# Kernel optimization log

Measured on AMD Instinct MI355X. Metric: run time of the kernel, lower is better.

## Reference

```python
import jax, jax.numpy as jnp
import numpy as np

N_NODES = 100000
N_EDGES = 1600000
IN_F, HID_F, OUT_F = 128, 128, 64


def gcn_conv(x, edge_index, W, b):
    # x: [N, Fin]; W: [Fout, Fin] (torch Linear layout); b: [Fout]
    h = x @ W.T + b  # [N, Fout]
    src, dst = edge_index[0], edge_index[1]
    n = x.shape[0]
    # in-degree via scatter-add of ones on dst (matches torch code)
    deg = jax.ops.segment_sum(jnp.ones(src.shape[0], dtype=h.dtype), dst, num_segments=n)
    deg_inv_sqrt = jnp.where(deg > 0, deg ** -0.5, 0.0)
    w = deg_inv_sqrt[src] * deg_inv_sqrt[dst]  # edge_weight defaults to ones
    msg = w[:, None] * h[src]  # [E, Fout] gather + scale
    return jax.ops.segment_sum(msg, dst, num_segments=n)  # scatter-add aggregate


def setup_inputs() -> dict:
    key = jax.random.key(0)
    k1, k2, k3, k4 = jax.random.split(key, 4)
    x = jax.random.normal(k1, (N_NODES, IN_F), dtype=jnp.float32)
    edge_index = jax.random.randint(k2, (2, N_EDGES), 0, N_NODES, dtype=jnp.int64)
    # xavier-uniform-like weights, zero bias (torch Linear layout [out, in])
    lim1 = float(np.sqrt(6.0 / (IN_F + HID_F)))
    lim2 = float(np.sqrt(6.0 / (HID_F + OUT_F)))
    W1 = jax.random.uniform(k3, (HID_F, IN_F), jnp.float32, -lim1, lim1)
    W2 = jax.random.uniform(k4, (OUT_F, HID_F), jnp.float32, -lim2, lim2)
    b1 = jnp.zeros((HID_F,), jnp.float32)
    b2 = jnp.zeros((OUT_F,), jnp.float32)
    return {"x": x, "edge_index": edge_index, "W1": W1, "b1": b1, "W2": W2, "b2": b2}


def reference(x, edge_index, W1, b1, W2, b2):
    # layer 1 + relu (dropout is identity in eval mode)
    h = jax.nn.relu(gcn_conv(x, edge_index, W1, b1))
    # final layer, no activation
    return gcn_conv(h, edge_index, W2, b2)
```

## Files before the change

### kernel.cpp

```cpp
#include <hip/hip_runtime.h>

constexpr int FIN    = 128;
constexpr int LOG_RB = 7;
constexpr int RB     = 1 << LOG_RB;
constexpr int BMAX   = 1024;
constexpr int CAP    = 8192;
constexpr int CHUNK  = 4096;

typedef _Float16 half8 __attribute__((ext_vector_type(8)));
typedef float    f32x4 __attribute__((ext_vector_type(4)));

__global__ __launch_bounds__(1024) void init_gcur_kernel(int* __restrict__ gcur, int B) {
    int i = blockIdx.x * 1024 + threadIdx.x;
    if (i < B) gcur[i] = i * CAP;
}

__global__ __launch_bounds__(256) void bucket_scatter_kernel(
    const int* __restrict__ src, const int* __restrict__ dst,
    int* __restrict__ gcur, unsigned* __restrict__ gEdges, int E, int B)
{
    __shared__ int lhist[BMAX];
    __shared__ int lbase[BMAX];
    __shared__ int lcur[BMAX];
    const int e0 = blockIdx.x * CHUNK;
    const int e1 = min(e0 + CHUNK, E);
    for (int i = threadIdx.x; i < B; i += 256) { lhist[i] = 0; lcur[i] = 0; }
    __syncthreads();
    for (int e = e0 + threadIdx.x; e < e1; e += 256)
        atomicAdd(&lhist[dst[e] >> LOG_RB], 1);
    __syncthreads();
    for (int i = threadIdx.x; i < B; i += 256) {
        int c = lhist[i];
        if (c) lbase[i] = atomicAdd(&gcur[i], c);
    }
    __syncthreads();
    for (int e = e0 + threadIdx.x; e < e1; e += 256) {
        int d = dst[e];
        int b = d >> LOG_RB;
        int pos = lbase[b] + atomicAdd(&lcur[b], 1);
        if (pos < (b + 1) * CAP)
            gEdges[pos] = ((unsigned)src[e] << LOG_RB) | (unsigned)(d & (RB - 1));
    }
}

__global__ __launch_bounds__(256) void finalize_kernel(
    const unsigned* __restrict__ gEdges, const int* __restrict__ gcur,
    int* __restrict__ rbeg, int* __restrict__ rend, float* __restrict__ dis,
    int* __restrict__ esrc, int N)
{
    __shared__ int h[RB];
    __shared__ int excl[RB];
    __shared__ int cur[RB];
    const int b = blockIdx.x;
    const int base = b * CAP;
    int cnt = gcur[b] - base;
    if (cnt > CAP) cnt = CAP;
    const int node0 = b << LOG_RB;
    if (threadIdx.x < RB) h[threadIdx.x] = 0;
    __syncthreads();
    for (int i = threadIdx.x; i < cnt; i += 256)
        atomicAdd(&h[gEdges[base + i] & (RB - 1)], 1);
    __syncthreads();
    if (threadIdx.x < RB) excl[threadIdx.x] = h[threadIdx.x];
    __syncthreads();
    for (int off = 1; off < RB; off <<= 1) {
        int u = 0;
        if (threadIdx.x < RB && threadIdx.x >= off) u = excl[threadIdx.x - off];
        __syncthreads();
        if (threadIdx.x < RB) excl[threadIdx.x] += u;
        __syncthreads();
    }
    if (threadIdx.x < RB) {
        int c  = h[threadIdx.x];
        int ex = excl[threadIdx.x] - c;
        cur[threadIdx.x] = ex;
        int node = node0 + threadIdx.x;
        if (node < N) {
            rbeg[node] = base + ex;
            rend[node] = base + ex + c;
            dis[node]  = c > 0 ? rsqrtf((float)c) : 0.0f;
        }
    }
    __syncthreads();
    for (int i = threadIdx.x; i < cnt; i += 256) {
        unsigned p = gEdges[base + i];
        int dl = (int)(p & (RB - 1));
        int pos = base + atomicAdd(&cur[dl], 1);
        esrc[pos] = (int)(p >> LOG_RB);
    }
}

__global__ __launch_bounds__(256) void linear1_kernel(
    const float* __restrict__ X, const float* __restrict__ W,
    const float* __restrict__ Bv, const float* __restrict__ dis,
    _Float16* __restrict__ Y, int N)
{
    __shared__ __align__(16) _Float16 xs[64 * 128];
    const int tid  = threadIdx.x;
    const int wave = tid >> 6;
    const int lane = tid & 63;
    const int l15  = lane & 15;
    const int lhi  = lane >> 4;

    half8 wf[2][4];
    float bias[2];
    #pragma unroll
    for (int c = 0; c < 2; ++c) {
        int f = (wave * 2 + c) * 16 + l15;
        #pragma unroll
        for (int ks = 0; ks < 4; ++ks) {
            const float* wp = &W[f * 128 + ks * 32 + lhi * 8];
            float4 u0 = *(const float4*)wp;
            float4 u1 = *(const float4*)(wp + 4);
            half8 hh;
            hh[0] = (_Float16)u0.x; hh[1] = (_Float16)u0.y;
            hh[2] = (_Float16)u0.z; hh[3] = (_Float16)u0.w;
            hh[4] = (_Float16)u1.x; hh[5] = (_Float16)u1.y;
            hh[6] = (_Float16)u1.z; hh[7] = (_Float16)u1.w;
            wf[c][ks] = hh;
        }
        bias[c] = Bv[f];
    }

    const int nchunks = (N + 63) / 64;
    for (int ch = blockIdx.x; ch < nchunks; ch += gridDim.x) {
        const int n0 = ch * 64;
        __syncthreads();
        #pragma unroll
        for (int p = 0; p < 4; ++p) {
            int ci  = p * 256 + tid;
            int row = ci >> 4, c = ci & 15;
            int n   = n0 + row;
            int nc  = n < N ? n : N - 1;
            const float* xp = &X[(size_t)nc * 128 + c * 8];
            float4 u0 = *(const float4*)xp;
            float4 u1 = *(const float4*)(xp + 4);
            half8 hh;
            hh[0] = (_Float16)u0.x; hh[1] = (_Float16)u0.y;
            hh[2] = (_Float16)u0.z; hh[3] = (_Float16)u0.w;
            hh[4] = (_Float16)u1.x; hh[5] = (_Float16)u1.y;
            hh[6] = (_Float16)u1.z; hh[7] = (_Float16)u1.w;
            *(half8*)&xs[row * 128 + (c ^ (row & 7)) * 8] = hh;
        }
        __syncthreads();

        f32x4 acc[4][2];
        #pragma unroll
        for (int mt = 0; mt < 4; ++mt)
            #pragma unroll
            for (int c = 0; c < 2; ++c) {
                acc[mt][c][0] = bias[c]; acc[mt][c][1] = bias[c];
                acc[mt][c][2] = bias[c]; acc[mt][c][3] = bias[c];
            }

        #pragma unroll
        for (int mt = 0; mt < 4; ++mt) {
            int row = mt * 16 + l15;
            #pragma unroll
            for (int ks = 0; ks < 4; ++ks) {
                int c  = ks * 4 + lhi;
                half8 a = *(const half8*)&xs[row * 128 + (c ^ (row & 7)) * 8];
                #pragma unroll
                for (int c2 = 0; c2 < 2; ++c2)
                    acc[mt][c2] = __builtin_amdgcn_mfma_f32_16x16x32_f16(
                        a, wf[c2][ks], acc[mt][c2], 0, 0, 0);
            }
        }
        __syncthreads();
        #pragma unroll
        for (int mt = 0; mt < 4; ++mt)
            #pragma unroll
            for (int r = 0; r < 4; ++r) {
                int row = mt * 16 + lhi * 4 + r;
                int n   = n0 + row;
                int nc  = n < N ? n : N - 1;
                float dv = dis[nc];
                #pragma unroll
                for (int c2 = 0; c2 < 2; ++c2) {
                    int col = (wave * 2 + c2) * 16 + l15;
                    xs[row * 128 + col] = (_Float16)(dv * acc[mt][c2][r]);
                }
            }
        __syncthreads();
        #pragma unroll
        for (int p = 0; p < 4; ++p) {
            int ci  = p * 256 + tid;
            int row = ci >> 4, c = ci & 15;
            int n   = n0 + row;
            if (n < N)
                *(half8*)&Y[(size_t)n * 128 + c * 8] = *(const half8*)&xs[row * 128 + c * 8];
        }
    }
}

__global__ __launch_bounds__(256) void agg_lin2_kernel(
    const _Float16* __restrict__ H, const int* __restrict__ rbeg,
    const int* __restrict__ rend, const int* __restrict__ esrc,
    const float* __restrict__ dis, const float* __restrict__ W2,
    const float* __restrict__ b2, _Float16* __restrict__ h2, int N)
{
    __shared__ __align__(16) _Float16 tile[16 * 128];
    const int tid  = threadIdx.x;
    const int wave = tid >> 6;
    const int lane = tid & 63;
    const int l15  = lane & 15;
    const int lhi  = lane >> 4;
    const int rlane = tid & 15;
    const int rrow  = tid >> 4;

    half8 wf[4];
    float bias;
    {
        int f = wave * 16 + l15;
        #pragma unroll
        for (int ks = 0; ks < 4; ++ks) {
            const float* wp = &W2[f * 128 + ks * 32 + lhi * 8];
            float4 u0 = *(const float4*)wp;
            float4 u1 = *(const float4*)(wp + 4);
            half8 hh;
            hh[0] = (_Float16)u0.x; hh[1] = (_Float16)u0.y;
            hh[2] = (_Float16)u0.z; hh[3] = (_Float16)u0.w;
            hh[4] = (_Float16)u1.x; hh[5] = (_Float16)u1.y;
            hh[6] = (_Float16)u1.z; hh[7] = (_Float16)u1.w;
            wf[ks] = hh;
        }
        bias = b2[f];
    }

    const int nchunks = (N + 15) / 16;
    for (int ch = blockIdx.x; ch < nchunks; ch += gridDim.x) {
        const int d0 = ch * 16;
        const int d  = d0 + rrow;
        __syncthreads();

        float a0[8] = {0,0,0,0,0,0,0,0}, a1[8] = {0,0,0,0,0,0,0,0};
        int beg = 0, end = 0;
        float wd = 0.0f;
        if (d < N) { beg = rbeg[d]; end = rend[d]; wd = dis[d]; }
        int e = beg;
        for (; e + 4 <= end; e += 4) {
            int s0 = esrc[e], s1 = esrc[e+1], s2 = esrc[e+2], s3 = esrc[e+3];
            half8 v0 = *(const half8*)&H[(size_t)s0 * 128 + rlane * 8];
            half8 v1 = *(const half8*)&H[(size_t)s1 * 128 + rlane * 8];
            half8 v2 = *(const half8*)&H[(size_t)s2 * 128 + rlane * 8];
            half8 v3 = *(const half8*)&H[(size_t)s3 * 128 + rlane * 8];
            #pragma unroll
            for (int j = 0; j < 8; ++j) {
                a0[j] += (float)v0[j]; a1[j] += (float)v1[j];
                a0[j] += (float)v2[j]; a1[j] += (float)v3[j];
            }
        }
        for (; e < end; ++e) {
            int s0 = esrc[e];
            half8 v0 = *(const half8*)&H[(size_t)s0 * 128 + rlane * 8];
            #pragma unroll
            for (int j = 0; j < 8; ++j) a0[j] += (float)v0[j];
        }
        half8 hv;
        #pragma unroll
        for (int j = 0; j < 8; ++j) {
            float t = wd * (a0[j] + a1[j]);
            hv[j] = (_Float16)fmaxf(t, 0.0f);
        }
        *(half8*)&tile[rrow * 128 + (rlane ^ (rrow & 7)) * 8] = hv;
        __syncthreads();

        f32x4 acc;
        acc[0] = bias; acc[1] = bias; acc[2] = bias; acc[3] = bias;
        #pragma unroll
        for (int ks = 0; ks < 4; ++ks) {
            int c = ks * 4 + lhi;
            half8 a = *(const half8*)&tile[l15 * 128 + (c ^ (l15 & 7)) * 8];
            acc = __builtin_amdgcn_mfma_f32_16x16x32_f16(a, wf[ks], acc, 0, 0, 0);
        }
        #pragma unroll
        for (int r = 0; r < 4; ++r) {
            int row = lhi * 4 + r;
            int n   = d0 + row;
            if (n < N)
                h2[(size_t)n * 64 + wave * 16 + l15] = (_Float16)(dis[n] * acc[r]);
        }
    }
}

__global__ __launch_bounds__(256) void aggregate64h_kernel(
    const _Float16* __restrict__ H, const int* __restrict__ rbeg,
    const int* __restrict__ rend, const int* __restrict__ esrc,
    const float* __restrict__ dis, float* __restrict__ OUT, int N)
{
    const int lane = threadIdx.x & 7;
    const int d = blockIdx.x * 32 + (threadIdx.x >> 3);
    if (d >= N) return;
    const int beg = rbeg[d], end = rend[d];
    float a0[8] = {0,0,0,0,0,0,0,0}, a1[8] = {0,0,0,0,0,0,0,0};
    int e = beg;
    for (; e + 4 <= end; e += 4) {
        int s0 = esrc[e], s1 = esrc[e+1], s2 = esrc[e+2], s3 = esrc[e+3];
        half8 v0 = *(const half8*)&H[(size_t)s0 * 64 + lane * 8];
        half8 v1 = *(const half8*)&H[(size_t)s1 * 64 + lane * 8];
        half8 v2 = *(const half8*)&H[(size_t)s2 * 64 + lane * 8];
        half8 v3 = *(const half8*)&H[(size_t)s3 * 64 + lane * 8];
        #pragma unroll
        for (int j = 0; j < 8; ++j) {
            a0[j] += (float)v0[j]; a1[j] += (float)v1[j];
            a0[j] += (float)v2[j]; a1[j] += (float)v3[j];
        }
    }
    for (; e < end; ++e) {
        int s0 = esrc[e];
        half8 v0 = *(const half8*)&H[(size_t)s0 * 64 + lane * 8];
        #pragma unroll
        for (int j = 0; j < 8; ++j) a0[j] += (float)v0[j];
    }
    float w = dis[d];
    float4 o0, o1;
    o0.x = w * (a0[0] + a1[0]); o0.y = w * (a0[1] + a1[1]);
    o0.z = w * (a0[2] + a1[2]); o0.w = w * (a0[3] + a1[3]);
    o1.x = w * (a0[4] + a1[4]); o1.y = w * (a0[5] + a1[5]);
    o1.z = w * (a0[6] + a1[6]); o1.w = w * (a0[7] + a1[7]);
    float* p = &OUT[(size_t)d * 64 + lane * 8];
    *(float4*)p = o0;
    *(float4*)(p + 4) = o1;
}

template <int FOUT, bool RELU_IN>
__global__ __launch_bounds__(256) void linear_kernel(
    const float* __restrict__ X, const float* __restrict__ W,
    const float* __restrict__ Bv, float* __restrict__ Y, int N)
{
    constexpr int TX = FOUT / 4;
    constexpr int TY = 256 / TX;
    constexpr int NB = 4 * TY;
    constexpr int QMASK = TX - 1;
    __shared__ float ws[FIN * FOUT];
    __shared__ float xs[NB * FIN];
    const int tid = threadIdx.x;
    const int tx  = tid % TX;
    const int ty  = tid / TX;
    for (int i = tid; i < FOUT * FIN; i += 256) {
        int f = i >> 7;
        int k = i & (FIN - 1);
        int q = f >> 2, r = f & 3;
        int qq = q ^ (k & QMASK);
        ws[k * FOUT + qq * 4 + r] = W[i];
    }
    const float4 bv = *(const float4*)&Bv[tx * 4];
    const int nchunks = (N + NB - 1) / NB;
    for (int c = blockIdx.x; c < nchunks; c += gridDim.x) {
        const int n0 = c * NB;
        __syncthreads();
        constexpr int V4 = FIN / 4;
        for (int i4 = tid; i4 < NB * V4; i4 += 256) {
            int row = i4 / V4, c4 = i4 % V4;
            int n = n0 + row;
            int nc = n < N ? n : N - 1;
            float4 v = *(const float4*)&X[(long long)nc * FIN + c4 * 4];
            if (RELU_IN) {
                v.x = fmaxf(v.x, 0.0f); v.y = fmaxf(v.y, 0.0f);
                v.z = fmaxf(v.z, 0.0f); v.w = fmaxf(v.w, 0.0f);
            }
            *(float4*)&xs[row * FIN + c4 * 4] = v;
        }
        __syncthreads();
        float acc[4][4];
        #pragma unroll
        for (int j = 0; j < 4; ++j) {
            acc[j][0] = bv.x; acc[j][1] = bv.y; acc[j][2] = bv.z; acc[j][3] = bv.w;
        }
        #pragma unroll 2
        for (int k = 0; k < FIN; k += 4) {
            float w[4][4];
            #pragma unroll
            for (int kk = 0; kk < 4; ++kk) {
                int kr = k + kk;
                float4 t = *(const float4*)&ws[kr * FOUT + ((tx ^ (kr & QMASK)) << 2)];
                w[kk][0] = t.x; w[kk][1] = t.y; w[kk][2] = t.z; w[kk][3] = t.w;
            }
            float xr[4][4];
            #pragma unroll
            for (int j = 0; j < 4; ++j) {
                float4 t = *(const float4*)&xs[(ty * 4 + j) * FIN + k];
                xr[j][0] = t.x; xr[j][1] = t.y; xr[j][2] = t.z; xr[j][3] = t.w;
            }
            #pragma unroll
            for (int j = 0; j < 4; ++j)
                #pragma unroll
                for (int kk = 0; kk < 4; ++kk) {
                    acc[j][0] = fmaf(xr[j][kk], w[kk][0], acc[j][0]);
                    acc[j][1] = fmaf(xr[j][kk], w[kk][1], acc[j][1]);
                    acc[j][2] = fmaf(xr[j][kk], w[kk][2], acc[j][2]);
                    acc[j][3] = fmaf(xr[j][kk], w[kk][3], acc[j][3]);
                }
        }
        #pragma unroll
        for (int j = 0; j < 4; ++j) {
            int n = n0 + ty * 4 + j;
            if (n < N) {
                float4 o;
                o.x = acc[j][0]; o.y = acc[j][1]; o.z = acc[j][2]; o.w = acc[j][3];
                *(float4*)&Y[(long long)n * FOUT + tx * 4] = o;
            }
        }
    }
}

template <int LOGF>
__global__ __launch_bounds__(256) void scatter_kernel(
    const float* __restrict__ H, const int* __restrict__ src,
    const int* __restrict__ dst, const float* __restrict__ dis,
    float* __restrict__ OUT, int E)
{
    constexpr int F = 1 << LOGF;
    const long long total  = (long long)E << LOGF;
    const long long stride = (long long)gridDim.x * blockDim.x;
    for (long long i = (long long)blockIdx.x * blockDim.x + threadIdx.x;
         i < total; i += stride) {
        int e = (int)(i >> LOGF);
        int f = (int)i & (F - 1);
        int s = src[e];
        int d = dst[e];
        float w = dis[s] * dis[d];
        atomicAdd(&OUT[d * F + f], w * H[s * F + f]);
    }
}

__global__ __launch_bounds__(256) void dis_inplace_kernel(float* __restrict__ deg, int N) {
    int i = blockIdx.x * 256 + threadIdx.x;
    if (i < N) {
        float d = deg[i];
        deg[i] = d > 0.0f ? rsqrtf(d) : 0.0f;
    }
}

__global__ __launch_bounds__(256) void deg_kernel_f(const int* __restrict__ dst,
                                                    float* __restrict__ deg, int E) {
    int stride = gridDim.x * 256;
    for (int i = blockIdx.x * 256 + threadIdx.x; i < E; i += stride)
        atomicAdd(&deg[dst[i]], 1.0f);
}

static inline size_t align512(size_t x) { return (x + 511) & ~(size_t)511; }

extern "C" void kernel_launch(void* const* d_in, const int* in_sizes, int n_in,
                              void* d_out, int out_size, void* d_ws, size_t ws_size,
                              hipStream_t stream)
{
    const float* x  = (const float*)d_in[0];
    const int*   ei = (const int*)d_in[1];
    const float* W1 = (const float*)d_in[2];
    const float* b1 = (const float*)d_in[3];
    const float* W2 = (const float*)d_in[4];
    const float* b2 = (const float*)d_in[5];

    const int N = in_sizes[0] / FIN;
    const int E = in_sizes[1] / 2;
    const int* src = ei;
    const int* dst = ei + E;
    float* out = (float*)d_out;
    char* wsb = (char*)d_ws;

    const int B = (N + RB - 1) / RB;

    size_t hreg = (size_t)N * 128 * 2;
    size_t areg = (size_t)B * CAP * 4;
    size_t h1sz = hreg > areg ? hreg : areg;
    size_t o = 0;
    int*      gcur  = (int*)(wsb + o);      o = align512(o + (size_t)BMAX * 4);
    int*      rbeg  = (int*)(wsb + o);      o = align512(o + (size_t)N * 4);
    int*      rendp = (int*)(wsb + o);      o = align512(o + (size_t)N * 4);
    float*    dis   = (float*)(wsb + o);    o = align512(o + (size_t)N * 4);
    int*      esrcA = (int*)(wsb + o);      o = align512(o + areg);
    _Float16* h1    = (_Float16*)(wsb + o); o = align512(o + h1sz);
    _Float16* h2    = (_Float16*)(wsb + o); o = align512(o + (size_t)N * 64 * 2);
    size_t need = o;
    unsigned* gEdges = (unsigned*)h1;

    if (ws_size >= need && B <= BMAX) {
        init_gcur_kernel<<<(B + 1023) / 1024, 1024, 0, stream>>>(gcur, B);
        bucket_scatter_kernel<<<(E + CHUNK - 1) / CHUNK, 256, 0, stream>>>(
            src, dst, gcur, gEdges, E, B);
        finalize_kernel<<<B, 256, 0, stream>>>(gEdges, gcur, rbeg, rendp, dis, esrcA, N);

        linear1_kernel<<<512, 256, 0, stream>>>(x, W1, b1, dis, h1, N);
        agg_lin2_kernel<<<2048, 256, 0, stream>>>(h1, rbeg, rendp, esrcA, dis,
                                                  W2, b2, h2, N);
        aggregate64h_kernel<<<(N + 31) / 32, 256, 0, stream>>>(h2, rbeg, rendp,
                                                               esrcA, dis, out, N);
    } else {
        float* deg  = (float*)wsb;
        size_t off  = align512((size_t)N * 4);
        float* fh1  = (float*)(wsb + off);
        float* fagg = fh1 + (size_t)N * FIN;
        float* fh2  = fh1;

        hipMemsetAsync(deg,  0, (size_t)N * 4, stream);
        hipMemsetAsync(fagg, 0, (size_t)N * FIN * 4, stream);
        hipMemsetAsync(out,  0, (size_t)N * 64 * 4, stream);

        deg_kernel_f<<<2048, 256, 0, stream>>>(dst, deg, E);
        dis_inplace_kernel<<<(N + 255) / 256, 256, 0, stream>>>(deg, N);

        linear_kernel<128, false><<<512, 256, 0, stream>>>(x, W1, b1, fh1, N);
        scatter_kernel<7><<<8192, 256, 0, stream>>>(fh1, src, dst, deg, fagg, E);
        linear_kernel<64, true><<<512, 256, 0, stream>>>(fagg, W2, b2, fh2, N);
        scatter_kernel<6><<<8192, 256, 0, stream>>>(fh2, src, dst, deg, out, E);
    }
}
```

Measured before the change: 179.6 us.

## Make agg_lin2 wave-independent per 16-row chunk; register-cache bucket scatter dst

```diff
diff --git a/kernel.cpp b/kernel.cpp
--- a/kernel.cpp
+++ b/kernel.cpp
@@ -5,7 +5,7 @@
 constexpr int RB     = 1 << LOG_RB;
 constexpr int BMAX   = 1024;
 constexpr int CAP    = 8192;
-constexpr int CHUNK  = 4096;
+constexpr int CHUNK  = 2048;
 
 typedef _Float16 half8 __attribute__((ext_vector_type(8)));
 typedef float    f32x4 __attribute__((ext_vector_type(4)));
@@ -23,23 +23,30 @@
     __shared__ int lbase[BMAX];
     __shared__ int lcur[BMAX];
     const int e0 = blockIdx.x * CHUNK;
-    const int e1 = min(e0 + CHUNK, E);
     for (int i = threadIdx.x; i < B; i += 256) { lhist[i] = 0; lcur[i] = 0; }
     __syncthreads();
-    for (int e = e0 + threadIdx.x; e < e1; e += 256)
-        atomicAdd(&lhist[dst[e] >> LOG_RB], 1);
+    int dreg[8];
+    #pragma unroll
+    for (int k = 0; k < 8; ++k) {
+        int e = e0 + k * 256 + threadIdx.x;
+        dreg[k] = (e < E) ? dst[e] : -1;
+        if (dreg[k] >= 0) atomicAdd(&lhist[dreg[k] >> LOG_RB], 1);
+    }
     __syncthreads();
     for (int i = threadIdx.x; i < B; i += 256) {
         int c = lhist[i];
         if (c) lbase[i] = atomicAdd(&gcur[i], c);
     }
     __syncthreads();
-    for (int e = e0 + threadIdx.x; e < e1; e += 256) {
-        int d = dst[e];
-        int b = d >> LOG_RB;
-        int pos = lbase[b] + atomicAdd(&lcur[b], 1);
-        if (pos < (b + 1) * CAP)
-            gEdges[pos] = ((unsigned)src[e] << LOG_RB) | (unsigned)(d & (RB - 1));
+    #pragma unroll
+    for (int k = 0; k < 8; ++k) {
+        int e = e0 + k * 256 + threadIdx.x;
+        if (dreg[k] >= 0) {
+            int b = dreg[k] >> LOG_RB;
+            int pos = lbase[b] + atomicAdd(&lcur[b], 1);
+            if (pos < (b + 1) * CAP)
+                gEdges[pos] = ((unsigned)src[e] << LOG_RB) | (unsigned)(dreg[k] & (RB - 1));
+        }
     }
 }
 
@@ -199,19 +206,18 @@
     const float* __restrict__ dis, const float* __restrict__ W2,
     const float* __restrict__ b2, _Float16* __restrict__ h2, int N)
 {
-    __shared__ __align__(16) _Float16 tile[16 * 128];
+    __shared__ __align__(16) _Float16 tile[4][16 * 128];
     const int tid  = threadIdx.x;
     const int wave = tid >> 6;
     const int lane = tid & 63;
     const int l15  = lane & 15;
     const int lhi  = lane >> 4;
-    const int rlane = tid & 15;
-    const int rrow  = tid >> 4;
-
-    half8 wf[4];
-    float bias;
-    {
-        int f = wave * 16 + l15;
+
+    half8 wf[4][4];
+    float bias[4];
+    #pragma unroll
+    for (int ct = 0; ct < 4; ++ct) {
+        int f = ct * 16 + l15;
         #pragma unroll
         for (int ks = 0; ks < 4; ++ks) {
             const float* wp = &W2[f * 128 + ks * 32 + lhi * 8];
@@ -222,63 +228,78 @@
             hh[2] = (_Float16)u0.z; hh[3] = (_Float16)u0.w;
             hh[4] = (_Float16)u1.x; hh[5] = (_Float16)u1.y;
             hh[6] = (_Float16)u1.z; hh[7] = (_Float16)u1.w;
-            wf[ks] = hh;
-        }
-        bias = b2[f];
-    }
+            wf[ct][ks] = hh;
+        }
+        bias[ct] = b2[f];
+    }
+    _Float16* mytile = tile[wave];
 
     const int nchunks = (N + 15) / 16;
-    for (int ch = blockIdx.x; ch < nchunks; ch += gridDim.x) {
+    const int wstep   = gridDim.x * 4;
+    for (int ch = blockIdx.x * 4 + wave; ch < nchunks; ch += wstep) {
         const int d0 = ch * 16;
-        const int d  = d0 + rrow;
-        __syncthreads();
-
-        float a0[8] = {0,0,0,0,0,0,0,0}, a1[8] = {0,0,0,0,0,0,0,0};
-        int beg = 0, end = 0;
-        float wd = 0.0f;
-        if (d < N) { beg = rbeg[d]; end = rend[d]; wd = dis[d]; }
-        int e = beg;
-        for (; e + 4 <= end; e += 4) {
-            int s0 = esrc[e], s1 = esrc[e+1], s2 = esrc[e+2], s3 = esrc[e+3];
-            half8 v0 = *(const half8*)&H[(size_t)s0 * 128 + rlane * 8];
-            half8 v1 = *(const half8*)&H[(size_t)s1 * 128 + rlane * 8];
-            half8 v2 = *(const half8*)&H[(size_t)s2 * 128 + rlane * 8];
-            half8 v3 = *(const half8*)&H[(size_t)s3 * 128 + rlane * 8];
-            #pragma unroll
-            for (int j = 0; j < 8; ++j) {
-                a0[j] += (float)v0[j]; a1[j] += (float)v1[j];
-                a0[j] += (float)v2[j]; a1[j] += (float)v3[j];
-            }
-        }
-        for (; e < end; ++e) {
-            int s0 = esrc[e];
-            half8 v0 = *(const half8*)&H[(size_t)s0 * 128 + rlane * 8];
-            #pragma unroll
-            for (int j = 0; j < 8; ++j) a0[j] += (float)v0[j];
-        }
-        half8 hv;
-        #pragma unroll
-        for (int j = 0; j < 8; ++j) {
-            float t = wd * (a0[j] + a1[j]);
-            hv[j] = (_Float16)fmaxf(t, 0.0f);
-        }
-        *(half8*)&tile[rrow * 128 + (rlane ^ (rrow & 7)) * 8] = hv;
-        __syncthreads();
-
-        f32x4 acc;
-        acc[0] = bias; acc[1] = bias; acc[2] = bias; acc[3] = bias;
+
+        #pragma unroll
+        for (int j = 0; j < 4; ++j) {
+            const int r = lhi * 4 + j;
+            const int d = d0 + r;
+            float a0[8] = {0,0,0,0,0,0,0,0}, a1[8] = {0,0,0,0,0,0,0,0};
+            int beg = 0, end = 0;
+            float wd = 0.0f;
+            if (d < N) { beg = rbeg[d]; end = rend[d]; wd = dis[d]; }
+            int e = beg;
+            for (; e + 4 <= end; e += 4) {
+                int s0 = esrc[e], s1 = esrc[e+1], s2 = esrc[e+2], s3 = esrc[e+3];
+                half8 v0 = *(const half8*)&H[(size_t)s0 * 128 + l15 * 8];
+                half8 v1 = *(const half8*)&H[(size_t)s1 * 128 + l15 * 8];
+                half8 v2 = *(const half8*)&H[(size_t)s2 * 128 + l15 * 8];
+                half8 v3 = *(const half8*)&H[(size_t)s3 * 128 + l15 * 8];
+                #pragma unroll
+                for (int q = 0; q < 8; ++q) {
+                    a0[q] += (float)v0[q]; a1[q] += (float)v1[q];
+                    a0[q] += (float)v2[q]; a1[q] += (float)v3[q];
+                }
+            }
+            for (; e < end; ++e) {
+                int s0 = esrc[e];
+                half8 v0 = *(const half8*)&H[(size_t)s0 * 128 + l15 * 8];
+                #pragma unroll
+                for (int q = 0; q < 8; ++q) a0[q] += (float)v0[q];
+            }
+            half8 hv;
+            #pragma unroll
+            for (int q = 0; q < 8; ++q) {
+                float t = wd * (a0[q] + a1[q]);
+                hv[q] = (_Float16)fmaxf(t, 0.0f);
+            }
+            *(half8*)&mytile[r * 128 + ((l15 ^ (r & 7)) * 8)] = hv;
+        }
+
+        f32x4 acc[4];
+        #pragma unroll
+        for (int ct = 0; ct < 4; ++ct) {
+            acc[ct][0] = bias[ct]; acc[ct][1] = bias[ct];
+            acc[ct][2] = bias[ct]; acc[ct][3] = bias[ct];
+        }
         #pragma unroll
         for (int ks = 0; ks < 4; ++ks) {
             int c = ks * 4 + lhi;
-            half8 a = *(const half8*)&tile[l15 * 128 + (c ^ (l15 & 7)) * 8];
-            acc = __builtin_amdgcn_mfma_f32_16x16x32_f16(a, wf[ks], acc, 0, 0, 0);
-        }
-        #pragma unroll
-        for (int r = 0; r < 4; ++r) {
-            int row = lhi * 4 + r;
-            int n   = d0 + row;
-            if (n < N)
-                h2[(size_t)n * 64 + wave * 16 + l15] = (_Float16)(dis[n] * acc[r]);
+            half8 a = *(const half8*)&mytile[l15 * 128 + ((c ^ (l15 & 7)) * 8)];
+            #pragma unroll
+            for (int ct = 0; ct < 4; ++ct)
+                acc[ct] = __builtin_amdgcn_mfma_f32_16x16x32_f16(
+                    a, wf[ct][ks], acc[ct], 0, 0, 0);
+        }
+
+        #pragma unroll
+        for (int r2 = 0; r2 < 4; ++r2) {
+            int n = d0 + lhi * 4 + r2;
+            if (n < N) {
+                float dv = dis[n];
+                #pragma unroll
+                for (int ct = 0; ct < 4; ++ct)
+                    h2[(size_t)n * 64 + ct * 16 + l15] = (_Float16)(dv * acc[ct][r2]);
+            }
         }
     }
 }
@@ -482,8 +503,12 @@
         finalize_kernel<<<B, 256, 0, stream>>>(gEdges, gcur, rbeg, rendp, dis, esrcA, N);
 
         linear1_kernel<<<512, 256, 0, stream>>>(x, W1, b1, dis, h1, N);
-        agg_lin2_kernel<<<2048, 256, 0, stream>>>(h1, rbeg, rendp, esrcA, dis,
-                                                  W2, b2, h2, N);
+        {
+            int nchunks = (N + 15) / 16;
+            int grid = (nchunks + 3) / 4;
+            agg_lin2_kernel<<<grid, 256, 0, stream>>>(h1, rbeg, rendp, esrcA, dis,
+                                                      W2, b2, h2, N);
+        }
         aggregate64h_kernel<<<(N + 31) / 32, 256, 0, stream>>>(h2, rbeg, rendp,
                                                                esrcA, dis, out, N);
     } else {
```

Result: slower. 238.6 us (+32.8%).

## Split fused aggregate+linear2 kernel into standalone aggregation and tiled MFMA linear

Applied to the files above, without the earlier changes.

```diff
diff --git a/kernel.cpp b/kernel.cpp
--- a/kernel.cpp
+++ b/kernel.cpp
@@ -193,20 +193,60 @@
     }
 }
 
-__global__ __launch_bounds__(256) void agg_lin2_kernel(
+__global__ __launch_bounds__(256) void aggregate128h_kernel(
     const _Float16* __restrict__ H, const int* __restrict__ rbeg,
     const int* __restrict__ rend, const int* __restrict__ esrc,
-    const float* __restrict__ dis, const float* __restrict__ W2,
-    const float* __restrict__ b2, _Float16* __restrict__ h2, int N)
-{
-    __shared__ __align__(16) _Float16 tile[16 * 128];
+    const float* __restrict__ dis, _Float16* __restrict__ OUT, int N)
+{
+    const int lane = threadIdx.x & 15;
+    const int d = blockIdx.x * 16 + (threadIdx.x >> 4);
+    if (d >= N) return;
+    const int beg = rbeg[d], end = rend[d];
+    float acc[4][8];
+    #pragma unroll
+    for (int u = 0; u < 4; ++u)
+        #pragma unroll
+        for (int j = 0; j < 8; ++j) acc[u][j] = 0.0f;
+    int e = beg;
+    for (; e + 4 <= end; e += 4) {
+        int s0 = esrc[e], s1 = esrc[e+1], s2 = esrc[e+2], s3 = esrc[e+3];
+        half8 v0 = *(const half8*)&H[(size_t)s0 * 128 + lane * 8];
+        half8 v1 = *(const half8*)&H[(size_t)s1 * 128 + lane * 8];
+        half8 v2 = *(const half8*)&H[(size_t)s2 * 128 + lane * 8];
+        half8 v3 = *(const half8*)&H[(size_t)s3 * 128 + lane * 8];
+        #pragma unroll
+        for (int j = 0; j < 8; ++j) {
+            acc[0][j] += (float)v0[j]; acc[1][j] += (float)v1[j];
+            acc[2][j] += (float)v2[j]; acc[3][j] += (float)v3[j];
+        }
+    }
+    for (; e < end; ++e) {
+        int s0 = esrc[e];
+        half8 v0 = *(const half8*)&H[(size_t)s0 * 128 + lane * 8];
+        #pragma unroll
+        for (int j = 0; j < 8; ++j) acc[0][j] += (float)v0[j];
+    }
+    float w = dis[d];
+    half8 o;
+    #pragma unroll
+    for (int j = 0; j < 8; ++j) {
+        float t = w * ((acc[0][j] + acc[1][j]) + (acc[2][j] + acc[3][j]));
+        o[j] = (_Float16)fmaxf(t, 0.0f);
+    }
+    *(half8*)&OUT[(size_t)d * 128 + lane * 8] = o;
+}
+
+__global__ __launch_bounds__(256) void lin2_kernel(
+    const _Float16* __restrict__ Xh, const float* __restrict__ W,
+    const float* __restrict__ Bv, const float* __restrict__ dis,
+    _Float16* __restrict__ Y, int N)
+{
+    __shared__ __align__(16) _Float16 xs[64 * 128];
     const int tid  = threadIdx.x;
     const int wave = tid >> 6;
     const int lane = tid & 63;
     const int l15  = lane & 15;
     const int lhi  = lane >> 4;
-    const int rlane = tid & 15;
-    const int rrow  = tid >> 4;
 
     half8 wf[4];
     float bias;
@@ -214,7 +254,7 @@
         int f = wave * 16 + l15;
         #pragma unroll
         for (int ks = 0; ks < 4; ++ks) {
-            const float* wp = &W2[f * 128 + ks * 32 + lhi * 8];
+            const float* wp = &W[f * 128 + ks * 32 + lhi * 8];
             float4 u0 = *(const float4*)wp;
             float4 u1 = *(const float4*)(wp + 4);
             half8 hh;
@@ -224,61 +264,59 @@
             hh[6] = (_Float16)u1.z; hh[7] = (_Float16)u1.w;
             wf[ks] = hh;
         }
-        bias = b2[f];
-    }
-
-    const int nchunks = (N + 15) / 16;
+        bias = Bv[f];
+    }
+
+    const int nchunks = (N + 63) / 64;
     for (int ch = blockIdx.x; ch < nchunks; ch += gridDim.x) {
-        const int d0 = ch * 16;
-        const int d  = d0 + rrow;
-        __syncthreads();
-
-        float a0[8] = {0,0,0,0,0,0,0,0}, a1[8] = {0,0,0,0,0,0,0,0};
-        int beg = 0, end = 0;
-        float wd = 0.0f;
-        if (d < N) { beg = rbeg[d]; end = rend[d]; wd = dis[d]; }
-        int e = beg;
-        for (; e + 4 <= end; e += 4) {
-            int s0 = esrc[e], s1 = esrc[e+1], s2 = esrc[e+2], s3 = esrc[e+3];
-            half8 v0 = *(const half8*)&H[(size_t)s0 * 128 + rlane * 8];
-            half8 v1 = *(const half8*)&H[(size_t)s1 * 128 + rlane * 8];
-            half8 v2 = *(const half8*)&H[(size_t)s2 * 128 + rlane * 8];
-            half8 v3 = *(const half8*)&H[(size_t)s3 * 128 + rlane * 8];
-            #pragma unroll
-            for (int j = 0; j < 8; ++j) {
-                a0[j] += (float)v0[j]; a1[j] += (float)v1[j];
-                a0[j] += (float)v2[j]; a1[j] += (float)v3[j];
-            }
-        }
-        for (; e < end; ++e) {
-            int s0 = esrc[e];
-            half8 v0 = *(const half8*)&H[(size_t)s0 * 128 + rlane * 8];
-            #pragma unroll
-            for (int j = 0; j < 8; ++j) a0[j] += (float)v0[j];
-        }
-        half8 hv;
-        #pragma unroll
-        for (int j = 0; j < 8; ++j) {
-            float t = wd * (a0[j] + a1[j]);
-            hv[j] = (_Float16)fmaxf(t, 0.0f);
-        }
-        *(half8*)&tile[rrow * 128 + (rlane ^ (rrow & 7)) * 8] = hv;
-        __syncthreads();
-
-        f32x4 acc;
-        acc[0] = bias; acc[1] = bias; acc[2] = bias; acc[3] = bias;
-        #pragma unroll
-        for (int ks = 0; ks < 4; ++ks) {
-            int c = ks * 4 + lhi;
-            half8 a = *(const half8*)&tile[l15 * 128 + (c ^ (l15 & 7)) * 8];
-            acc = __builtin_amdgcn_mfma_f32_16x16x32_f16(a, wf[ks], acc, 0, 0, 0);
-        }
-        #pragma unroll
-        for (int r = 0; r < 4; ++r) {
-            int row = lhi * 4 + r;
-            int n   = d0 + row;
+        const int n0 = ch * 64;
+        __syncthreads();
+        #pragma unroll
+        for (int p = 0; p < 4; ++p) {
+            int ci  = p * 256 + tid;
+            int row = ci >> 4, c = ci & 15;
+            int n   = n0 + row;
+            int nc  = n < N ? n : N - 1;
+            half8 hh = *(const half8*)&Xh[(size_t)nc * 128 + c * 8];
+            *(half8*)&xs[row * 128 + (c ^ (row & 7)) * 8] = hh;
+        }
+        __syncthreads();
+
+        f32x4 acc[4];
+        #pragma unroll
+        for (int mt = 0; mt < 4; ++mt) {
+            acc[mt][0] = bias; acc[mt][1] = bias;
+            acc[mt][2] = bias; acc[mt][3] = bias;
+        }
+        #pragma unroll
+        for (int mt = 0; mt < 4; ++mt) {
+            int row = mt * 16 + l15;
+            #pragma unroll
+            for (int ks = 0; ks < 4; ++ks) {
+                int c  = ks * 4 + lhi;
+                half8 a = *(const half8*)&xs[row * 128 + (c ^ (row & 7)) * 8];
+                acc[mt] = __builtin_amdgcn_mfma_f32_16x16x32_f16(a, wf[ks], acc[mt], 0, 0, 0);
+            }
+        }
+        __syncthreads();
+        #pragma unroll
+        for (int mt = 0; mt < 4; ++mt)
+            #pragma unroll
+            for (int r = 0; r < 4; ++r) {
+                int row = mt * 16 + lhi * 4 + r;
+                int n   = n0 + row;
+                int nc  = n < N ? n : N - 1;
+                float dv = dis[nc];
+                xs[row * 64 + wave * 16 + l15] = (_Float16)(dv * acc[mt][r]);
+            }
+        __syncthreads();
+        #pragma unroll
+        for (int p = 0; p < 2; ++p) {
+            int ci  = p * 256 + tid;
+            int row = ci >> 3, c = ci & 7;
+            int n   = n0 + row;
             if (n < N)
-                h2[(size_t)n * 64 + wave * 16 + l15] = (_Float16)(dis[n] * acc[r]);
+                *(half8*)&Y[(size_t)n * 64 + c * 8] = *(const half8*)&xs[row * 64 + c * 8];
         }
     }
 }
@@ -471,6 +509,7 @@
     float*    dis   = (float*)(wsb + o);    o = align512(o + (size_t)N * 4);
     int*      esrcA = (int*)(wsb + o);      o = align512(o + areg);
     _Float16* h1    = (_Float16*)(wsb + o); o = align512(o + h1sz);
+    _Float16* agg1  = (_Float16*)(wsb + o); o = align512(o + (size_t)N * 128 * 2);
     _Float16* h2    = (_Float16*)(wsb + o); o = align512(o + (size_t)N * 64 * 2);
     size_t need = o;
     unsigned* gEdges = (unsigned*)h1;
@@ -482,8 +521,9 @@
         finalize_kernel<<<B, 256, 0, stream>>>(gEdges, gcur, rbeg, rendp, dis, esrcA, N);
 
         linear1_kernel<<<512, 256, 0, stream>>>(x, W1, b1, dis, h1, N);
-        agg_lin2_kernel<<<2048, 256, 0, stream>>>(h1, rbeg, rendp, esrcA, dis,
-                                                  W2, b2, h2, N);
+        aggregate128h_kernel<<<(N + 15) / 16, 256, 0, stream>>>(h1, rbeg, rendp,
+                                                                esrcA, dis, agg1, N);
+        lin2_kernel<<<512, 256, 0, stream>>>(agg1, W2, b2, dis, h2, N);
         aggregate64h_kernel<<<(N + 31) / 32, 256, 0, stream>>>(h2, rbeg, rendp,
                                                                esrcA, dis, out, N);
     } else {
```

After: 175.9 us. 2.1% less time.
